# Kernel optimization log

Hardware: AMD Instinct MI355X
Metric: run time of the kernel (lower is better)

## Reference

```python
import jax, jax.numpy as jnp
import numpy as np

B, IN_CH, HID, OUT_CH, GH, GW = 16, 64, 128, 64, 64, 64


def grid_edges(h, w):
    # torch_geometric.utils.grid: 8-neighborhood + self-loop, edge = (node, node+offset)
    idx = np.arange(h * w).reshape(h, w)
    rows, cols = [], []
    for dr in (-1, 0, 1):
        for dc in (-1, 0, 1):
            node = idx[max(0, -dr):h - max(0, dr), max(0, -dc):w - max(0, dc)]
            nb = idx[max(0, dr):h + min(0, dr) or None, max(0, dc):w + min(0, dc) or None]
            rows.append(node.ravel())
            cols.append(nb.ravel())
    return np.stack([np.concatenate(rows), np.concatenate(cols)])


def setup_inputs() -> dict:
    key = jax.random.key(0)
    ks = jax.random.split(key, 32)
    def rn(i, shape, scale=0.05):
        return jax.random.normal(ks[i], shape, dtype=jnp.float32) * scale
    e = grid_edges(GH, GW)                                   # (2, E)
    offs = (np.arange(B) * (GH * GW)).reshape(B, 1, 1)
    ei = (e[None] + offs).transpose(1, 0, 2).reshape(2, -1)  # (2, B*E) batched offsets
    return {
        "x": rn(0, (B, IN_CH, GH, GW), 1.0),
        "cW1": rn(1, (HID, IN_CH, 3, 3)), "cb1": rn(2, (HID,)),
        "cW2": rn(3, (IN_CH, HID, 3, 3)), "cb2": rn(4, (IN_CH,)),
        "q1W": rn(5, (HID, IN_CH)), "q1b": rn(6, (HID,)),
        "k1W": rn(7, (HID, IN_CH)), "k1b": rn(8, (HID,)),
        "v1W": rn(9, (HID, IN_CH)), "v1b": rn(10, (HID,)),
        "s1W": rn(11, (HID, IN_CH)), "s1b": rn(12, (HID,)),
        "q2W": rn(13, (IN_CH, HID)), "q2b": rn(14, (IN_CH,)),
        "k2W": rn(15, (IN_CH, HID)), "k2b": rn(16, (IN_CH,)),
        "v2W": rn(17, (IN_CH, HID)), "v2b": rn(18, (IN_CH,)),
        "s2W": rn(19, (IN_CH, HID)), "s2b": rn(20, (IN_CH,)),
        "fW1": rn(21, (HID, 2 * IN_CH, 3, 3)), "fb1": rn(22, (HID,)),
        "fW2": rn(23, (OUT_CH, HID, 3, 3)), "fb2": rn(24, (OUT_CH,)),
        "edge_index": jnp.asarray(ei, dtype=jnp.int32),
    }


def gelu(x):
    return jax.nn.gelu(x, approximate=False)


def sn_conv(x, W, b):
    # spectral_norm: power iteration on (O, I*k*k) matrix; u,v detached, grad through sigma
    O = W.shape[0]
    Wm = W.reshape(O, -1)
    u = jnp.ones((O,), W.dtype) / jnp.sqrt(jnp.asarray(O, W.dtype))
    for _ in range(3):
        v = Wm.T @ u
        v = v / (jnp.linalg.norm(v) + 1e-12)
        u = Wm @ v
        u = u / (jnp.linalg.norm(u) + 1e-12)
    u = jax.lax.stop_gradient(u)
    v = jax.lax.stop_gradient(v)
    sigma = u @ (Wm @ v)
    Wn = W / sigma
    xp = jnp.pad(x, ((0, 0), (0, 0), (1, 1), (1, 1)), mode='edge')  # replicate padding
    y = jax.lax.conv_general_dilated(xp, Wn, (1, 1), 'VALID',
                                     dimension_numbers=('NCHW', 'OIHW', 'NCHW'))
    return y + b[None, :, None, None]


def tconv(x, src, dst, N, heads, qW, qb, kW, kb, vW, vb, sW, sb):
    # PyG TransformerConv (concat=True, root_weight=True, no edge features)
    d = qW.shape[0] // heads
    q = (x @ qW.T + qb)[dst].reshape(-1, heads, d)
    k = (x @ kW.T + kb)[src].reshape(-1, heads, d)
    v = (x @ vW.T + vb)[src].reshape(-1, heads, d)
    alpha = (q * k).sum(-1) / jnp.sqrt(jnp.asarray(d, x.dtype))      # (E, heads)
    m = jax.ops.segment_max(alpha, dst, num_segments=N)               # scatter-softmax
    a = jnp.exp(alpha - m[dst])
    s = jax.ops.segment_sum(a, dst, num_segments=N)
    a = a / (s[dst] + 1e-16)
    out = jax.ops.segment_sum(a[:, :, None] * v, dst, num_segments=N)  # (N, heads, d)
    return out.reshape(N, heads * d) + x @ sW.T + sb


def reference(x, cW1, cb1, cW2, cb2, q1W, q1b, k1W, k1b, v1W, v1b, s1W, s1b,
              q2W, q2b, k2W, k2b, v2W, v2b, s2W, s2b, fW1, fb1, fW2, fb2, edge_index):
    Bb, C, Hc, Wc = x.shape
    N = Bb * Hc * Wc
    # CNN branch (DoubleConvBlock)
    x1 = gelu(sn_conv(gelu(sn_conv(x, cW1, cb1)), cW2, cb2))
    # GCN branch
    xf = x.transpose(0, 2, 3, 1).reshape(N, C)
    src, dst = edge_index[0], edge_index[1]
    h = gelu(tconv(xf, src, dst, N, 8, q1W, q1b, k1W, k1b, v1W, v1b, s1W, s1b))
    h = gelu(tconv(h, src, dst, N, 1, q2W, q2b, k2W, k2b, v2W, v2b, s2W, s2b))
    x2 = h.reshape(Bb, Hc, Wc, -1).transpose(0, 3, 1, 2)
    # Fusion
    xc = jnp.concatenate([x1, x2], axis=1)
    return gelu(sn_conv(gelu(sn_conv(xc, fW1, fb1)), fW2, fb2))
```

## Files before the change

### kernel.cpp

```cpp
#include <hip/hip_runtime.h>
#include <hip/hip_bf16.h>

typedef unsigned int  u32;
typedef unsigned short u16;
typedef __attribute__((ext_vector_type(8))) short bf16x8;
typedef __attribute__((ext_vector_type(4))) float f32x4;
typedef __attribute__((ext_vector_type(4))) u32 u32x4;

#define NPIX 65536

constexpr size_t SIG   = 0;
constexpr size_t B1OFF = 256;
constexpr size_t B2OFF = B1OFF + 2048;
constexpr size_t WC1   = B2OFF + 1024;
constexpr size_t WC2   = WC1 + 147456;
constexpr size_t WF1   = WC2 + 147456;
constexpr size_t WF2   = WF1 + 294912;
constexpr size_t WP1   = WF2 + 147456;
constexpr size_t WP2   = WP1 + 65536;
constexpr size_t XB    = WP2 + 65536;
constexpr size_t HBUF  = XB + 8388608;
constexpr size_t QKVS2 = HBUF + 16777216;
constexpr size_t XC    = QKVS2 + 33554432;
constexpr size_t QKVS1 = XC + 16777216;
constexpr size_t TBUF  = QKVS1 + 16777216;
constexpr size_t GRAM  = QKVS1 + 67108864;

__device__ __forceinline__ float gelu_f(float v) {
    float xa = fabsf(v) * 0.70710678118654752f;
    float t  = __fdividef(1.0f, fmaf(0.3275911f, xa, 1.0f));
    float poly = t * fmaf(t, fmaf(t, fmaf(t, fmaf(t, 1.061405429f, -1.453152027f),
                   1.421413741f), -0.284496736f), 0.254829592f);
    float erfv = 1.0f - poly * __expf(-xa * xa);
    erfv = copysignf(erfv, v);
    return 0.5f * v * (1.0f + erfv);
}
__device__ __forceinline__ u16 f2bf(float f) {
    __hip_bfloat16 b = __float2bfloat16(f);
    return *reinterpret_cast<u16*>(&b);
}
__device__ __forceinline__ float blo(u32 u) {
    union { u32 i; float f; } x; x.i = u << 16; return x.f;
}
__device__ __forceinline__ float bhi(u32 u) {
    union { u32 i; float f; } x; x.i = u & 0xffff0000u; return x.f;
}
__device__ __forceinline__ u32 packbf(float a, float b) {
    return (u32)f2bf(a) | ((u32)f2bf(b) << 16);
}
__device__ __forceinline__ void g2l16(const void* g, void* l) {
    __builtin_amdgcn_global_load_lds(
        (const __attribute__((address_space(1))) u32*)g,
        (__attribute__((address_space(3))) u32*)l, 16, 0, 0);
}

__device__ float block_sum(float vv, float* red) {
    #pragma unroll
    for (int m = 1; m < 64; m <<= 1) vv += __shfl_xor(vv, m);
    int tid = threadIdx.x;
    __syncthreads();
    if ((tid & 63) == 0) red[tid >> 6] = vv;
    __syncthreads();
    return red[0] + red[1] + red[2] + red[3];
}


__device__ void gram_body(int bid, char* smem,
                          const float* cW1, const float* cW2,
                          const float* fW1, const float* fW2, float* Gall) {
    const float* W; int O, K, wsel, tile;
    if (bid < 64)       { W = cW1; O = 128; K = 576;  wsel = 0; tile = bid; }
    else if (bid < 80)  { W = cW2; O = 64;  K = 1152; wsel = 1; tile = bid - 64; }
    else if (bid < 144) { W = fW1; O = 128; K = 1152; wsel = 2; tile = bid - 80; }
    else                { W = fW2; O = 64;  K = 1152; wsel = 3; tile = bid - 144; }
    int ntiles = O >> 4;
    int ti0 = (tile / ntiles) << 4, tj0 = (tile % ntiles) << 4;
    float (*Wi)[33] = (float(*)[33])smem;
    float (*Wj)[33] = (float(*)[33])(smem + 16 * 33 * 4);
    int tid = threadIdx.x;
    int ti = tid >> 4, tj = tid & 15;
    int r = tid >> 5, c = tid & 31;
    float acc = 0.f;
    for (int k0 = 0; k0 < K; k0 += 32) {
        Wi[r][c]     = W[(size_t)(ti0 + r) * K + k0 + c];
        Wi[r + 8][c] = W[(size_t)(ti0 + r + 8) * K + k0 + c];
        Wj[r][c]     = W[(size_t)(tj0 + r) * K + k0 + c];
        Wj[r + 8][c] = W[(size_t)(tj0 + r + 8) * K + k0 + c];
        __syncthreads();
        #pragma unroll
        for (int k = 0; k < 32; ++k)
            acc += Wi[ti][k] * Wj[tj][k];
        __syncthreads();
    }
    Gall[wsel * 16384 + (ti0 + ti) * 128 + (tj0 + tj)] = acc;
}

__device__ void convert_body(int bid, char* smem,
                             const float* __restrict__ x, u16* __restrict__ xb) {
    float (*tile)[65] = (float(*)[65])smem;
    int b = bid >> 6, y = bid & 63;
    int tid = threadIdx.x;
    #pragma unroll
    for (int i = 0; i < 16; ++i) {
        int c = (tid >> 6) + i * 4;
        tile[c][tid & 63] = x[(((size_t)b * 64 + c) << 12) + (y << 6) + (tid & 63)];
    }
    __syncthreads();
    #pragma unroll
    for (int i = 0; i < 16; ++i) {
        int idx = tid + i * 256;
        int p = idx >> 6, c = idx & 63;
        xb[(((size_t)b << 12) + (y << 6) + p) * 64 + c] = f2bf(tile[c][p]);
    }
}

__device__ void prep_proj_body(int bid,
               const float* q1W, const float* k1W, const float* v1W, const float* s1W,
               const float* q2W, const float* k2W, const float* v2W, const float* s2W,
               const float* q1b, const float* k1b, const float* v1b, const float* s1b,
               const float* q2b, const float* k2b, const float* v2b, const float* s2b,
               u16* wp1, u16* wp2, float* b1, float* b2) {
    const float* W1[4] = {q1W, k1W, v1W, s1W};
    const float* W2[4] = {q2W, k2W, v2W, s2W};
    const float* Bb1[4] = {q1b, k1b, v1b, s1b};
    const float* Bb2[4] = {q2b, k2b, v2b, s2b};
    int idx = bid * 256 + threadIdx.x;
    if (idx < 32768) {
        int w = idx >> 13, r = idx & 8191;
        wp1[(size_t)w * 8192 + r] = f2bf(W1[w][r]);
    } else if (idx < 65536) {
        int j = idx - 32768; int w = j >> 13, r = j & 8191;
        wp2[(size_t)w * 8192 + r] = f2bf(W2[w][r]);
    } else if (idx < 66048) {
        int j = idx - 65536; int w = j >> 7; b1[j] = Bb1[w][j & 127];
    } else if (idx < 66304) {
        int j = idx - 66048; int w = j >> 6; b2[j] = Bb2[w][j & 63];
    }
}

__device__ void prep_conv_w_body(int bx, int wsel,
                 const float* __restrict__ cW1, const float* __restrict__ cW2,
                 const float* __restrict__ fW1, const float* __restrict__ fW2,
                 const float* __restrict__ sig,
                 u16* wc1, u16* wc2, u16* wf1, u16* wf2) {
    const float* src; u16* dst; int O, C;
    switch (wsel) {
        case 0:  src = cW1; dst = wc1; O = 128; C = 64;  break;
        case 1:  src = cW2; dst = wc2; O = 64;  C = 128; break;
        case 2:  src = fW1; dst = wf1; O = 128; C = 128; break;
        default: src = fW2; dst = wf2; O = 64;  C = 128; break;
    }
    int idx = bx * 256 + threadIdx.x;
    if (idx >= O * C * 9) return;
    int o = idx / (C * 9);
    int rem = idx - o * (C * 9);
    int ci = rem / 9, tap = rem - ci * 9;
    float v = src[idx] / sig[wsel];
    dst[(size_t)o * (C * 9) + tap * C + ci] = f2bf(v);
}

template<int TAPS, int CC, int BN, int OUTM>
__device__ void mm_body(int bx, int by, char* smem,
               const u16* __restrict__ A, const u16* __restrict__ Bw,
               const float* __restrict__ bias, void* __restrict__ Cout,
               int ostride, int ocol0, int do_gelu) {
    constexpr int K = CC * TAPS;
    constexpr int NSTEP = TAPS;
    constexpr int NCH = CC / 8;
    constexpr int NKS = CC / 32;
    constexpr int NF = BN / 32;
    constexpr int HN = BN / 2;
    constexpr int RSTEP = 256 / NCH;
    constexpr int ALD = 128 / RSTEP;
    constexpr int BLD = BN / RSTEP;
    u16* Als = (u16*)smem;
    u16* Bls = (u16*)smem + 128 * CC;
    const int tid = threadIdx.x;
    const int w = tid >> 6;
    const int lane = tid & 63;
    const int m0 = bx * 128;
    const int nt0 = by * BN;
    const int wm = w >> 1, wn = w & 1;

    const int srow = tid / NCH;
    const int sslot = tid % NCH;
    const int csrc = ((sslot ^ (srow & (NCH - 1))) << 3);
    const u16* Bbase = Bw + (size_t)(nt0 + srow) * K + csrc;

    int offA[NKS][4], offB[NKS][NF];
    #pragma unroll
    for (int ks = 0; ks < NKS; ++ks) {
        #pragma unroll
        for (int mf = 0; mf < 4; ++mf) {
            int R = wm * 64 + mf * 16 + (lane & 15);
            int slot = (ks * 4 + (lane >> 4)) ^ (R & (NCH - 1));
            offA[ks][mf] = R * CC + slot * 8;
        }
        #pragma unroll
        for (int nf = 0; nf < NF; ++nf) {
            int Rb = wn * HN + nf * 16 + (lane & 15);
            int slot = (ks * 4 + (lane >> 4)) ^ (Rb & (NCH - 1));
            offB[ks][nf] = Rb * CC + slot * 8;
        }
    }

    f32x4 acc[4][NF];
    #pragma unroll
    for (int i = 0; i < 4; ++i)
        #pragma unroll
        for (int j = 0; j < NF; ++j) {
            f32x4 z = {0.f, 0.f, 0.f, 0.f};
            acc[i][j] = z;
        }

    #pragma unroll
    for (int kt = 0; kt < NSTEP; ++kt) {
        const int kk = kt * CC;
        const int dy = (TAPS == 9) ? (kt / 3 - 1) : 0;
        const int dx = (TAPS == 9) ? (kt % 3 - 1) : 0;
        #pragma unroll
        for (int i = 0; i < ALD; ++i) {
            const int m = m0 + srow + i * RSTEP;
            const u16* ga;
            if constexpr (TAPS == 9) {
                int yy = ((m >> 6) & 63) + dy; yy = min(max(yy, 0), 63);
                int xx = (m & 63) + dx;        xx = min(max(xx, 0), 63);
                ga = A + (size_t)((m & ~4095) | (yy << 6) | xx) * CC + csrc;
            } else {
                ga = A + (size_t)m * CC + csrc;
            }
            g2l16(ga, &Als[(srow + i * RSTEP) * CC + sslot * 8]);
        }
        #pragma unroll
        for (int i = 0; i < BLD; ++i)
            g2l16(Bbase + (size_t)i * RSTEP * K + kk,
                  &Bls[(srow + i * RSTEP) * CC + sslot * 8]);

        __syncthreads();

        #pragma unroll
        for (int ks = 0; ks < NKS; ++ks) {
            bf16x8 af[4];
            #pragma unroll
            for (int mf = 0; mf < 4; ++mf)
                af[mf] = *reinterpret_cast<const bf16x8*>(&Als[offA[ks][mf]]);
            #pragma unroll
            for (int nf = 0; nf < NF; ++nf) {
                bf16x8 bfv = *reinterpret_cast<const bf16x8*>(&Bls[offB[ks][nf]]);
                #pragma unroll
                for (int mf = 0; mf < 4; ++mf)
                    acc[mf][nf] = __builtin_amdgcn_mfma_f32_16x16x32_bf16(
                        af[mf], bfv, acc[mf][nf], 0, 0, 0);
            }
        }
        if (kt + 1 < NSTEP) __syncthreads();
    }

    #pragma unroll
    for (int mf = 0; mf < 4; ++mf) {
        int mrow = m0 + wm * 64 + mf * 16 + (lane >> 4) * 4;
        #pragma unroll
        for (int nf = 0; nf < NF; ++nf) {
            int col = nt0 + wn * HN + nf * 16 + (lane & 15);
            float bv = bias[col];
            if (OUTM == 0) {
                u16* Co = (u16*)Cout;
                #pragma unroll
                for (int j = 0; j < 4; ++j) {
                    float v = acc[mf][nf][j] + bv;
                    if (do_gelu) v = gelu_f(v);
                    Co[(size_t)(mrow + j) * ostride + ocol0 + col] = f2bf(v);
                }
            } else {
                float* Co = (float*)Cout;
                int b = m0 >> 12;
                int pixb = (mrow & 4095);
                f32x4 vv;
                #pragma unroll
                for (int j = 0; j < 4; ++j)
                    vv[j] = gelu_f(acc[mf][nf][j] + bv);
                *reinterpret_cast<f32x4*>(&Co[((size_t)(b * 64 + col)) * 4096 + pixb]) = vv;
            }
        }
    }
}

__device__ void attn1_body(int bid, const u16* __restrict__ qkvs,
                           u16* __restrict__ h) {
    const int tid = threadIdx.x;
    const int l16 = tid & 15;
    const int n = bid * 16 + (tid >> 4);
    const int y = (n >> 6) & 63, x = n & 63;
    const u32* qk = (const u32*)qkvs;
    const int nbase = (n << 8) + l16 * 4;

    u32x4 qp = *(const u32x4*)(qk + nbase);
    float q[8];
    #pragma unroll
    for (int i = 0; i < 4; ++i) { q[2*i] = blo(qp[i]); q[2*i+1] = bhi(qp[i]); }

    float al[9];
    float mx = -1e30f;
    #pragma unroll
    for (int e = 0; e < 9; ++e) {
        const int dy = e / 3 - 1, dx = e % 3 - 1;
        const bool valid = (unsigned)(y + dy) < 64u && (unsigned)(x + dx) < 64u;
        const int off = valid ? ((dy * 64 + dx) << 8) : 0;
        u32x4 kp = *(const u32x4*)(qk + nbase + off + 64);
        float p = 0.f;
        #pragma unroll
        for (int i = 0; i < 4; ++i) {
            p = fmaf(q[2*i],   blo(kp[i]), p);
            p = fmaf(q[2*i+1], bhi(kp[i]), p);
        }
        p += __shfl_xor(p, 1);
        al[e] = valid ? p * 0.25f : -1e30f;
        mx = fmaxf(mx, al[e]);
    }
    float s = 0.f;
    #pragma unroll
    for (int e = 0; e < 9; ++e) { al[e] = __expf(al[e] - mx); s += al[e]; }

    float o[8] = {0.f, 0.f, 0.f, 0.f, 0.f, 0.f, 0.f, 0.f};
    #pragma unroll
    for (int e = 0; e < 9; ++e) {
        const int dy = e / 3 - 1, dx = e % 3 - 1;
        const bool valid = (unsigned)(y + dy) < 64u && (unsigned)(x + dx) < 64u;
        const int off = valid ? ((dy * 64 + dx) << 8) : 0;
        u32x4 vp = *(const u32x4*)(qk + nbase + off + 128);
        const float a = al[e];
        #pragma unroll
        for (int i = 0; i < 4; ++i) {
            o[2*i]   = fmaf(a, blo(vp[i]), o[2*i]);
            o[2*i+1] = fmaf(a, bhi(vp[i]), o[2*i+1]);
        }
    }
    const float r = __fdividef(1.0f, s + 1e-16f);
    u32x4 sp = *(const u32x4*)(qk + nbase + 192);
    u32x4 res;
    #pragma unroll
    for (int i = 0; i < 4; ++i) {
        float h0 = gelu_f(fmaf(o[2*i],   r, blo(sp[i])));
        float h1 = gelu_f(fmaf(o[2*i+1], r, bhi(sp[i])));
        res[i] = packbf(h0, h1);
    }
    *(u32x4*)((u32*)h + (n << 6) + l16 * 4) = res;
}


__global__ __launch_bounds__(256)
void power_kernel(const float* __restrict__ Gall, float* __restrict__ sig) {
    int wsel = blockIdx.x;
    const float* G = Gall + wsel * 16384;
    const int O = (wsel == 0 || wsel == 2) ? 128 : 64;
    __shared__ float u[128], t[128], red[4];
    int tid = threadIdx.x;
    if (tid < O) u[tid] = 1.0f / sqrtf((float)O);
    __syncthreads();
    for (int it = 0; it < 3; ++it) {
        if (tid < O) {
            float s = 0.f;
            const float4* gr = reinterpret_cast<const float4*>(G + (size_t)tid * 128);
            for (int j = 0; j < O / 4; ++j) {
                float4 g = gr[j];
                s += g.x * u[4*j] + g.y * u[4*j+1] + g.z * u[4*j+2] + g.w * u[4*j+3];
            }
            t[tid] = s;
        }
        __syncthreads();
        float loc = (tid < O) ? t[tid] * t[tid] : 0.f;
        float nt = sqrtf(block_sum(loc, red));
        if (it == 2) {
            float locd = (tid < O) ? u[tid] * t[tid] : 0.f;
            float dot = block_sum(locd, red);
            if (tid == 0) sig[wsel] = nt / sqrtf(dot + 1e-24f);
        } else {
            if (tid < O) u[tid] = t[tid] / (nt + 1e-12f);
            __syncthreads();
        }
    }
}

__global__ __launch_bounds__(256)
void attn2_kernel(const u16* __restrict__ qkvs, u16* __restrict__ xc) {
    const int tid = threadIdx.x;
    const int l8 = tid & 7;
    const int n = blockIdx.x * 32 + (tid >> 3);
    const int y = (n >> 6) & 63, x = n & 63;
    const u32* qk = (const u32*)qkvs;
    const int nbase = (n << 7) + l8 * 4;

    u32x4 qp = *(const u32x4*)(qk + nbase);
    float q[8];
    #pragma unroll
    for (int i = 0; i < 4; ++i) { q[2*i] = blo(qp[i]); q[2*i+1] = bhi(qp[i]); }

    float al[9];
    float mx = -1e30f;
    #pragma unroll
    for (int e = 0; e < 9; ++e) {
        const int dy = e / 3 - 1, dx = e % 3 - 1;
        const bool valid = (unsigned)(y + dy) < 64u && (unsigned)(x + dx) < 64u;
        const int off = valid ? ((dy * 64 + dx) << 7) : 0;
        u32x4 kp = *(const u32x4*)(qk + nbase + off + 32);
        float p = 0.f;
        #pragma unroll
        for (int i = 0; i < 4; ++i) {
            p = fmaf(q[2*i],   blo(kp[i]), p);
            p = fmaf(q[2*i+1], bhi(kp[i]), p);
        }
        p += __shfl_xor(p, 1);
        p += __shfl_xor(p, 2);
        p += __shfl_xor(p, 4);
        al[e] = valid ? p * 0.125f : -1e30f;
        mx = fmaxf(mx, al[e]);
    }
    float s = 0.f;
    #pragma unroll
    for (int e = 0; e < 9; ++e) { al[e] = __expf(al[e] - mx); s += al[e]; }

    float o[8] = {0.f, 0.f, 0.f, 0.f, 0.f, 0.f, 0.f, 0.f};
    #pragma unroll
    for (int e = 0; e < 9; ++e) {
        const int dy = e / 3 - 1, dx = e % 3 - 1;
        const bool valid = (unsigned)(y + dy) < 64u && (unsigned)(x + dx) < 64u;
        const int off = valid ? ((dy * 64 + dx) << 7) : 0;
        u32x4 vp = *(const u32x4*)(qk + nbase + off + 64);
        const float a = al[e];
        #pragma unroll
        for (int i = 0; i < 4; ++i) {
            o[2*i]   = fmaf(a, blo(vp[i]), o[2*i]);
            o[2*i+1] = fmaf(a, bhi(vp[i]), o[2*i+1]);
        }
    }
    const float r = __fdividef(1.0f, s + 1e-16f);
    u32x4 sp = *(const u32x4*)(qk + nbase + 96);
    u32x4 res;
    #pragma unroll
    for (int i = 0; i < 4; ++i) {
        float h0 = gelu_f(fmaf(o[2*i],   r, blo(sp[i])));
        float h1 = gelu_f(fmaf(o[2*i+1], r, bhi(sp[i])));
        res[i] = packbf(h0, h1);
    }
    *(u32x4*)((u32*)xc + (n << 6) + 32 + l8 * 4) = res;
}

template<int TAPS, int CC, int BN, int OUTM>
__global__ __launch_bounds__(256)
void mm_kernel(const u16* __restrict__ A, const u16* __restrict__ Bw,
               const float* __restrict__ bias, void* __restrict__ Cout,
               int ostride, int ocol0, int do_gelu) {
    __shared__ __align__(16) char smem[(128 * CC + BN * CC) * 2];
    mm_body<TAPS, CC, BN, OUTM>(blockIdx.x, blockIdx.y, smem, A, Bw, bias, Cout,
                                ostride, ocol0, do_gelu);
}

__global__ __launch_bounds__(256)
void fuse_misc(const float* cW1, const float* cW2, const float* fW1,
               const float* fW2, float* Gall,
               const float* x, u16* xb,
               const float* q1W, const float* k1W, const float* v1W, const float* s1W,
               const float* q2W, const float* k2W, const float* v2W, const float* s2W,
               const float* q1b, const float* k1b, const float* v1b, const float* s1b,
               const float* q2b, const float* k2b, const float* v2b, const float* s2b,
               u16* wp1, u16* wp2, float* b1, float* b2) {
    __shared__ __align__(16) char smem[16640];
    int bid = blockIdx.x;
    if (bid < 1024)       convert_body(bid, smem, x, xb);
    else if (bid < 1184)  gram_body(bid - 1024, smem, cW1, cW2, fW1, fW2, Gall);
    else                  prep_proj_body(bid - 1184, q1W, k1W, v1W, s1W,
                                         q2W, k2W, v2W, s2W, q1b, k1b, v1b, s1b,
                                         q2b, k2b, v2b, s2b, wp1, wp2, b1, b2);
}

__global__ __launch_bounds__(256)
void fuse_p1_w(const u16* xb, const u16* wp1, const float* b1, u16* qkvs1,
               const float* cW1, const float* cW2, const float* fW1,
               const float* fW2, const float* sig,
               u16* wc1, u16* wc2, u16* wf1, u16* wf2) {
    __shared__ __align__(16) char smem[(128 * 64 + 128 * 64) * 2];
    int bid = blockIdx.x;
    if (bid < 2048)
        mm_body<1, 64, 128, 0>(bid & 511, bid >> 9, smem, xb, wp1, b1,
                               (void*)qkvs1, 512, 0, 0);
    else {
        int wk = bid - 2048;
        prep_conv_w_body(wk % 576, wk / 576, cW1, cW2, fW1, fW2, sig,
                         wc1, wc2, wf1, wf2);
    }
}

__global__ __launch_bounds__(256)
void fuse_c1_a1(const u16* xb, const u16* wc1, const float* cb1, u16* y1,
                const u16* qkvs1, u16* hbuf) {
    __shared__ __align__(16) char smem[(128 * 64 + 128 * 64) * 2];
    int bid = blockIdx.x;
    if (bid < 512)
        mm_body<9, 64, 128, 0>(bid, 0, smem, xb, wc1, cb1, (void*)y1, 128, 0, 1);
    else
        attn1_body(bid - 512, qkvs1, hbuf);
}

__global__ __launch_bounds__(256)
void fuse_c2_p2(const u16* y1, const u16* wc2, const float* cb2, u16* xc,
                const u16* hbuf, const u16* wp2, const float* b2, u16* qkvs2) {
    __shared__ __align__(16) char smem[(128 * 128 + 128 * 128) * 2];
    int bid = blockIdx.x;
    if (bid < 512)
        mm_body<9, 128, 64, 0>(bid, 0, smem, y1, wc2, cb2, (void*)xc, 128, 0, 1);
    else {
        int wk = bid - 512;
        mm_body<1, 128, 128, 0>(wk & 511, wk >> 9, smem, hbuf, wp2, b2,
                                (void*)qkvs2, 256, 0, 0);
    }
}

extern "C" void kernel_launch(void* const* d_in, const int* in_sizes, int n_in,
                              void* d_out, int out_size, void* d_ws, size_t ws_size,
                              hipStream_t stream) {
    const float* x   = (const float*)d_in[0];
    const float* cW1 = (const float*)d_in[1];
    const float* cb1 = (const float*)d_in[2];
    const float* cW2 = (const float*)d_in[3];
    const float* cb2 = (const float*)d_in[4];
    const float* q1W = (const float*)d_in[5];
    const float* q1b = (const float*)d_in[6];
    const float* k1W = (const float*)d_in[7];
    const float* k1b = (const float*)d_in[8];
    const float* v1W = (const float*)d_in[9];
    const float* v1b = (const float*)d_in[10];
    const float* s1W = (const float*)d_in[11];
    const float* s1b = (const float*)d_in[12];
    const float* q2W = (const float*)d_in[13];
    const float* q2b = (const float*)d_in[14];
    const float* k2W = (const float*)d_in[15];
    const float* k2b = (const float*)d_in[16];
    const float* v2W = (const float*)d_in[17];
    const float* v2b = (const float*)d_in[18];
    const float* s2W = (const float*)d_in[19];
    const float* s2b = (const float*)d_in[20];
    const float* fW1 = (const float*)d_in[21];
    const float* fb1 = (const float*)d_in[22];
    const float* fW2 = (const float*)d_in[23];
    const float* fb2 = (const float*)d_in[24];

    char* ws = (char*)d_ws;
    float* sig  = (float*)(ws + SIG);
    float* b1   = (float*)(ws + B1OFF);
    float* b2   = (float*)(ws + B2OFF);
    u16* wc1    = (u16*)(ws + WC1);
    u16* wc2    = (u16*)(ws + WC2);
    u16* wf1    = (u16*)(ws + WF1);
    u16* wf2    = (u16*)(ws + WF2);
    u16* wp1    = (u16*)(ws + WP1);
    u16* wp2    = (u16*)(ws + WP2);
    u16* xb     = (u16*)(ws + XB);
    u16* hbuf   = (u16*)(ws + HBUF);
    u16* qkvs2  = (u16*)(ws + QKVS2);
    u16* xc     = (u16*)(ws + XC);
    u16* qkvs1  = (u16*)(ws + QKVS1);
    u16* tbuf   = (u16*)(ws + TBUF);
    float* gram = (float*)(ws + GRAM);
    float* out  = (float*)d_out;
    u16* y1     = (u16*)d_out;

    fuse_misc<<<1444, 256, 0, stream>>>(cW1, cW2, fW1, fW2, gram, x, xb,
        q1W, k1W, v1W, s1W, q2W, k2W, v2W, s2W,
        q1b, k1b, v1b, s1b, q2b, k2b, v2b, s2b, wp1, wp2, b1, b2);
    power_kernel<<<4, 256, 0, stream>>>(gram, sig);
    fuse_p1_w<<<4352, 256, 0, stream>>>(xb, wp1, b1, qkvs1,
        cW1, cW2, fW1, fW2, sig, wc1, wc2, wf1, wf2);
    fuse_c1_a1<<<4608, 256, 0, stream>>>(xb, wc1, cb1, y1, qkvs1, hbuf);
    fuse_c2_p2<<<1536, 256, 0, stream>>>(y1, wc2, cb2, xc, hbuf, wp2, b2, qkvs2);
    attn2_kernel<<<NPIX / 32, 256, 0, stream>>>(qkvs2, xc);
    mm_kernel<9, 128, 128, 0><<<dim3(512, 1), 256, 0, stream>>>(
        xc, wf1, fb1, tbuf, 128, 0, 1);
    mm_kernel<9, 128, 64, 1><<<dim3(512, 1), 256, 0, stream>>>(
        tbuf, wf2, fb2, out, 0, 0, 1);
}
```

Baseline: 193.2 us.

## Reuse A tile across projection groups and stage attention K/V neighbors in LDS

Adds a projection GEMM body that loads each 128-row A tile into shared memory once and loops over all output column groups. This replaces separate blocks per group that each reloaded A, and it cuts the block counts for the two projection launches. The first attention layer now cooperatively loads the 3x18 halo of K and V rows for a 16-pixel strip into LDS and reads neighbors from there instead of from global memory. The cost is fewer, longer blocks with less parallelism, plus an extra sync and clamped halo loads.

```diff
diff --git a/kernel.cpp b/kernel.cpp
--- a/kernel.cpp
+++ b/kernel.cpp
@@ -285,14 +285,134 @@
     }
 }
 
-__device__ void attn1_body(int bid, const u16* __restrict__ qkvs,
+template<int CC, int BN, int NGRP>
+__device__ void proj_body(int bx, char* smem,
+               const u16* __restrict__ A, const u16* __restrict__ Bw,
+               const float* __restrict__ bias, u16* __restrict__ Cout,
+               int ostride) {
+    constexpr int NCH = CC / 8;
+    constexpr int NKS = CC / 32;
+    constexpr int NF = BN / 32;
+    constexpr int HN = BN / 2;
+    constexpr int RSTEP = 256 / NCH;
+    constexpr int ALD = 128 / RSTEP;
+    constexpr int BLD = BN / RSTEP;
+    u16* Als = (u16*)smem;
+    u16* Bls = (u16*)smem + 128 * CC;
+    const int tid = threadIdx.x;
+    const int w = tid >> 6;
+    const int lane = tid & 63;
+    const int m0 = bx * 128;
+    const int wm = w >> 1, wn = w & 1;
+
+    const int srow = tid / NCH;
+    const int sslot = tid % NCH;
+    const int csrc = ((sslot ^ (srow & (NCH - 1))) << 3);
+
+    #pragma unroll
+    for (int i = 0; i < ALD; ++i) {
+        const int m = m0 + srow + i * RSTEP;
+        g2l16(A + (size_t)m * CC + csrc,
+              &Als[(srow + i * RSTEP) * CC + sslot * 8]);
+    }
+
+    int offA[NKS][4], offB[NKS][NF];
+    #pragma unroll
+    for (int ks = 0; ks < NKS; ++ks) {
+        #pragma unroll
+        for (int mf = 0; mf < 4; ++mf) {
+            int R = wm * 64 + mf * 16 + (lane & 15);
+            int slot = (ks * 4 + (lane >> 4)) ^ (R & (NCH - 1));
+            offA[ks][mf] = R * CC + slot * 8;
+        }
+        #pragma unroll
+        for (int nf = 0; nf < NF; ++nf) {
+            int Rb = wn * HN + nf * 16 + (lane & 15);
+            int slot = (ks * 4 + (lane >> 4)) ^ (Rb & (NCH - 1));
+            offB[ks][nf] = Rb * CC + slot * 8;
+        }
+    }
+
+    #pragma unroll
+    for (int g = 0; g < NGRP; ++g) {
+        const u16* Bbase = Bw + (size_t)(g * BN + srow) * CC + csrc;
+        #pragma unroll
+        for (int i = 0; i < BLD; ++i)
+            g2l16(Bbase + (size_t)i * RSTEP * CC,
+                  &Bls[(srow + i * RSTEP) * CC + sslot * 8]);
+        __syncthreads();
+
+        f32x4 acc[4][NF];
+        #pragma unroll
+        for (int i = 0; i < 4; ++i)
+            #pragma unroll
+            for (int j = 0; j < NF; ++j) {
+                f32x4 z = {0.f, 0.f, 0.f, 0.f};
+                acc[i][j] = z;
+            }
+        #pragma unroll
+        for (int ks = 0; ks < NKS; ++ks) {
+            bf16x8 af[4];
+            #pragma unroll
+            for (int mf = 0; mf < 4; ++mf)
+                af[mf] = *reinterpret_cast<const bf16x8*>(&Als[offA[ks][mf]]);
+            #pragma unroll
+            for (int nf = 0; nf < NF; ++nf) {
+                bf16x8 bfv = *reinterpret_cast<const bf16x8*>(&Bls[offB[ks][nf]]);
+                #pragma unroll
+                for (int mf = 0; mf < 4; ++mf)
+                    acc[mf][nf] = __builtin_amdgcn_mfma_f32_16x16x32_bf16(
+                        af[mf], bfv, acc[mf][nf], 0, 0, 0);
+            }
+        }
+        #pragma unroll
+        for (int mf = 0; mf < 4; ++mf) {
+            int mrow = m0 + wm * 64 + mf * 16 + (lane >> 4) * 4;
+            #pragma unroll
+            for (int nf = 0; nf < NF; ++nf) {
+                int col = g * BN + wn * HN + nf * 16 + (lane & 15);
+                float bv = bias[col];
+                #pragma unroll
+                for (int j = 0; j < 4; ++j)
+                    Cout[(size_t)(mrow + j) * ostride + col] =
+                        f2bf(acc[mf][nf][j] + bv);
+            }
+        }
+        if (g + 1 < NGRP) __syncthreads();
+    }
+}
+
+__device__ void attn1_body(int bid, char* smem, const u16* __restrict__ qkvs,
                            u16* __restrict__ h) {
+    u16* KV = (u16*)smem;
     const int tid = threadIdx.x;
+    const int w = tid >> 6;
+    const int lane = tid & 63;
+    const int n0 = bid * 16;
+    const int imgb = n0 & ~4095;
+    const int y = (n0 >> 6) & 63;
+    const int x0 = n0 & 63;
+
+    for (int t = w; t < 27; t += 4) {
+        const int r = 4 * t + (lane >> 4);
+        const int isV = r >= 54;
+        const int rr = isV ? r - 54 : r;
+        const int ry = rr / 18, rx = rr - ry * 18;
+        const int yy = min(max(y + ry - 1, 0), 63);
+        const int xx = min(max(x0 - 1 + rx, 0), 63);
+        const u16* g = qkvs + (size_t)(imgb + (yy << 6) + xx) * 512
+                        + (isV ? 256 : 128) + (lane & 15) * 8;
+        g2l16(g, KV + t * 512);
+    }
+    __syncthreads();
+
     const int l16 = tid & 15;
-    const int n = bid * 16 + (tid >> 4);
-    const int y = (n >> 6) & 63, x = n & 63;
+    const int nn = tid >> 4;
+    const int n = n0 + nn;
+    const int x = x0 + nn;
     const u32* qk = (const u32*)qkvs;
     const int nbase = (n << 8) + l16 * 4;
+    const u32* Kl = (const u32*)KV;
 
     u32x4 qp = *(const u32x4*)(qk + nbase);
     float q[8];
@@ -305,8 +425,8 @@
     for (int e = 0; e < 9; ++e) {
         const int dy = e / 3 - 1, dx = e % 3 - 1;
         const bool valid = (unsigned)(y + dy) < 64u && (unsigned)(x + dx) < 64u;
-        const int off = valid ? ((dy * 64 + dx) << 8) : 0;
-        u32x4 kp = *(const u32x4*)(qk + nbase + off + 64);
+        const int rk = (dy + 1) * 18 + nn + dx + 1;
+        u32x4 kp = *(const u32x4*)(Kl + rk * 64 + l16 * 4);
         float p = 0.f;
         #pragma unroll
         for (int i = 0; i < 4; ++i) {
@@ -325,9 +445,8 @@
     #pragma unroll
     for (int e = 0; e < 9; ++e) {
         const int dy = e / 3 - 1, dx = e % 3 - 1;
-        const bool valid = (unsigned)(y + dy) < 64u && (unsigned)(x + dx) < 64u;
-        const int off = valid ? ((dy * 64 + dx) << 8) : 0;
-        u32x4 vp = *(const u32x4*)(qk + nbase + off + 128);
+        const int rk = (dy + 1) * 18 + nn + dx + 1;
+        u32x4 vp = *(const u32x4*)(Kl + (54 + rk) * 64 + l16 * 4);
         const float a = al[e];
         #pragma unroll
         for (int i = 0; i < 4; ++i) {
@@ -480,11 +599,10 @@
                u16* wc1, u16* wc2, u16* wf1, u16* wf2) {
     __shared__ __align__(16) char smem[(128 * 64 + 128 * 64) * 2];
     int bid = blockIdx.x;
-    if (bid < 2048)
-        mm_body<1, 64, 128, 0>(bid & 511, bid >> 9, smem, xb, wp1, b1,
-                               (void*)qkvs1, 512, 0, 0);
+    if (bid < 512)
+        proj_body<64, 128, 4>(bid, smem, xb, wp1, b1, qkvs1, 512);
     else {
-        int wk = bid - 2048;
+        int wk = bid - 512;
         prep_conv_w_body(wk % 576, wk / 576, cW1, cW2, fW1, fW2, sig,
                          wc1, wc2, wf1, wf2);
     }
@@ -498,7 +616,7 @@
     if (bid < 512)
         mm_body<9, 64, 128, 0>(bid, 0, smem, xb, wc1, cb1, (void*)y1, 128, 0, 1);
     else
-        attn1_body(bid - 512, qkvs1, hbuf);
+        attn1_body(bid - 512, smem, qkvs1, hbuf);
 }
 
 __global__ __launch_bounds__(256)
@@ -508,11 +626,8 @@
     int bid = blockIdx.x;
     if (bid < 512)
         mm_body<9, 128, 64, 0>(bid, 0, smem, y1, wc2, cb2, (void*)xc, 128, 0, 1);
-    else {
-        int wk = bid - 512;
-        mm_body<1, 128, 128, 0>(wk & 511, wk >> 9, smem, hbuf, wp2, b2,
-                                (void*)qkvs2, 256, 0, 0);
-    }
+    else
+        proj_body<128, 128, 2>(bid - 512, smem, hbuf, wp2, b2, qkvs2, 256);
 }
 
 extern "C" void kernel_launch(void* const* d_in, const int* in_sizes, int n_in,
@@ -568,10 +683,10 @@
         q1W, k1W, v1W, s1W, q2W, k2W, v2W, s2W,
         q1b, k1b, v1b, s1b, q2b, k2b, v2b, s2b, wp1, wp2, b1, b2);
     power_kernel<<<4, 256, 0, stream>>>(gram, sig);
-    fuse_p1_w<<<4352, 256, 0, stream>>>(xb, wp1, b1, qkvs1,
+    fuse_p1_w<<<2816, 256, 0, stream>>>(xb, wp1, b1, qkvs1,
         cW1, cW2, fW1, fW2, sig, wc1, wc2, wf1, wf2);
     fuse_c1_a1<<<4608, 256, 0, stream>>>(xb, wc1, cb1, y1, qkvs1, hbuf);
-    fuse_c2_p2<<<1536, 256, 0, stream>>>(y1, wc2, cb2, xc, hbuf, wp2, b2, qkvs2);
+    fuse_c2_p2<<<1024, 256, 0, stream>>>(y1, wc2, cb2, xc, hbuf, wp2, b2, qkvs2);
     attn2_kernel<<<NPIX / 32, 256, 0, stream>>>(qkvs2, xc);
     mm_kernel<9, 128, 128, 0><<<dim3(512, 1), 256, 0, stream>>>(
         xc, wf1, fb1, tbuf, 128, 0, 1);
```

New measurement: 189.0 us. 1.02x faster.
